# Performance work log

Hardware: AMD Instinct MI355X
Metric: run time of the kernel (lower is better)

Reference implementation:

```python
import jax, jax.numpy as jnp
import numpy as np
import math

B, T, E, H = 64, 256, 1024, 16
HD = E // H  # 64
EPS = 1e-5


def layernorm(x, g, b):
    mu = jnp.mean(x, axis=-1, keepdims=True)
    var = jnp.mean(jnp.square(x - mu), axis=-1, keepdims=True)
    return (x - mu) * jax.lax.rsqrt(var + EPS) * g + b


def setup_inputs() -> dict:
    key = jax.random.key(0)
    ks = jax.random.split(key, 10)
    s = 0.02
    return {
        "x": jax.random.normal(ks[0], (B, T, E), dtype=jnp.float32),
        "ln1_g": jnp.ones((E,), jnp.float32),
        "ln1_b": jnp.zeros((E,), jnp.float32),
        "wk": jax.random.normal(ks[1], (H, E, HD), jnp.float32) * s,
        "wq": jax.random.normal(ks[2], (H, E, HD), jnp.float32) * s,
        "wv": jax.random.normal(ks[3], (H, E, HD), jnp.float32) * s,
        "w_proj": jax.random.normal(ks[4], (E, E), jnp.float32) * s,
        "b_proj": jnp.zeros((E,), jnp.float32),
        "ln2_g": jnp.ones((E,), jnp.float32),
        "ln2_b": jnp.zeros((E,), jnp.float32),
        "w1": jax.random.normal(ks[5], (E, E), jnp.float32) * s,
        "b1": jnp.zeros((E,), jnp.float32),
        "w2": jax.random.normal(ks[6], (E, E), jnp.float32) * s,
        "b2": jnp.zeros((E,), jnp.float32),
    }


def reference(x, ln1_g, ln1_b, wk, wq, wv, w_proj, b_proj, ln2_g, ln2_b, w1, b1, w2, b2):
    # --- multi-head causal attention on LN1(x) ---
    h = layernorm(x, ln1_g, ln1_b)
    k = jnp.einsum('bte,hed->bhtd', h, wk)
    q = jnp.einsum('bte,hed->bhtd', h, wq)
    v = jnp.einsum('bte,hed->bhtd', h, wv)
    # NOTE: original computes k @ q^T (K.Q^T), not the standard Q.K^T -- kept faithful
    scores = jnp.einsum('bhtd,bhsd->bhts', k, q) / math.sqrt(HD)
    mask = jnp.tril(jnp.ones((T, T), dtype=bool))
    scores = jnp.where(mask, scores, -jnp.inf)
    attn_w = jax.nn.softmax(scores, axis=-1)  # dropout = identity in eval
    attn = jnp.einsum('bhts,bhsd->bhtd', attn_w, v)
    attn = attn.transpose(0, 2, 1, 3).reshape(B, T, E)  # concat heads
    x = x + attn @ w_proj + b_proj
    # --- feed-forward on LN2(x) ---
    h2 = layernorm(x, ln2_g, ln2_b)
    ff = jax.nn.relu(h2 @ w1 + b1) @ w2 + b2
    return x + ff
```

## Files before the change

### kernel.cpp

```cpp
#include <hip/hip_runtime.h>

typedef unsigned int u32;
typedef unsigned short u16;
typedef __attribute__((ext_vector_type(8))) short bf16x8;
typedef __attribute__((ext_vector_type(4))) float f32x4;

#define GLOBAL_AS __attribute__((address_space(1)))
#define LDS_AS    __attribute__((address_space(3)))

#define B_   64
#define T_   256
#define E_   1024
#define H_   16
#define HD_  64
#define NTOK (B_*T_)
#define K_   1024
#define LNEPS 1e-5f

__device__ __forceinline__ u16 f2bf(float f){
  u32 x = __float_as_uint(f);
  u32 r = x + 0x7fffu + ((x >> 16) & 1u);
  return (u16)(r >> 16);
}
__device__ __forceinline__ u16 f2bf_trunc(float f){
  return (u16)(__float_as_uint(f) >> 16);
}
__device__ __forceinline__ u32 pack2(float a, float b){
  return (u32)f2bf(a) | ((u32)f2bf(b) << 16);
}

__device__ __forceinline__ void gload16(const u16* g, u16* l){
  __builtin_amdgcn_global_load_lds((const GLOBAL_AS void*)g, (LDS_AS void*)l, 16, 0, 0);
}

__global__ __launch_bounds__(256) void ln_bf16_kernel(
    const float* __restrict__ x, const float* __restrict__ g,
    const float* __restrict__ b, u16* __restrict__ o)
{
  int lane  = threadIdx.x & 63;
  int token = (blockIdx.x << 2) + (threadIdx.x >> 6);
  const float4* xr = (const float4*)(x + (size_t)token * E_);
  float4 v[4];
  float s = 0.f, ss = 0.f;
  #pragma unroll
  for (int i = 0; i < 4; ++i){
    v[i] = xr[lane + 64 * i];
    s += v[i].x + v[i].y + v[i].z + v[i].w;
    ss = fmaf(v[i].x, v[i].x, fmaf(v[i].y, v[i].y,
         fmaf(v[i].z, v[i].z, fmaf(v[i].w, v[i].w, ss))));
  }
  #pragma unroll
  for (int off = 32; off > 0; off >>= 1){
    s  += __shfl_xor(s,  off);
    ss += __shfl_xor(ss, off);
  }
  float mu   = s * (1.f / E_);
  float var  = ss * (1.f / E_) - mu * mu;
  float rstd = rsqrtf(var + LNEPS);
  const float4* gr = (const float4*)g;
  const float4* br = (const float4*)b;
  uint2* orow = (uint2*)(o + (size_t)token * E_);
  #pragma unroll
  for (int i = 0; i < 4; ++i){
    float4 gg = gr[lane + 64 * i], bb = br[lane + 64 * i];
    float y0 = (v[i].x - mu) * rstd * gg.x + bb.x;
    float y1 = (v[i].y - mu) * rstd * gg.y + bb.y;
    float y2 = (v[i].z - mu) * rstd * gg.z + bb.z;
    float y3 = (v[i].w - mu) * rstd * gg.w + bb.w;
    orow[lane + 64 * i] = make_uint2(pack2(y0, y1), pack2(y2, y3));
  }
}

__global__ __launch_bounds__(256) void convq_kernel(
    const float* __restrict__ wk, const float* __restrict__ wq,
    const float* __restrict__ wv, u16* __restrict__ o)
{
  __shared__ float tile[64 * 68];
  const int zh = blockIdx.x, z = zh >> 4, h = zh & 15;
  const int k0 = blockIdx.y << 6;
  const float* w = (z == 0 ? wk : z == 1 ? wq : wv) + (size_t)h * (E_ * HD_);
  const int t = threadIdx.x;
  {
    int kr = t >> 2, d0 = (t & 3) << 4;
    const float4* src = (const float4*)(w + (size_t)(k0 + kr) * HD_ + d0);
    #pragma unroll
    for (int i = 0; i < 4; ++i)
      *(float4*)(tile + kr * 68 + d0 + 4 * i) = src[i];
  }
  __syncthreads();
  {
    const size_t nb32 = (size_t)zh * 32 + (k0 >> 5);
    #pragma unroll
    for (int u = 0; u < 2; ++u) {
      int cid = t * 2 + u;
      int dd = cid >> 3, kc = cid & 7;
      u32 wd[4];
      #pragma unroll
      for (int e2 = 0; e2 < 4; ++e2)
        wd[e2] = pack2(tile[(kc * 8 + 2 * e2) * 68 + dd],
                       tile[(kc * 8 + 2 * e2 + 1) * 68 + dd]);
      u16* dst = o + (nb32 + (kc >> 2)) * 2048 + (size_t)(dd >> 4) * 512
                   + (size_t)(((kc & 3) << 4) + (dd & 15)) * 8;
      *(uint4*)dst = make_uint4(wd[0], wd[1], wd[2], wd[3]);
    }
  }
}

__global__ __launch_bounds__(256) void convt3_kernel(
    const float* __restrict__ wp, const float* __restrict__ w1,
    const float* __restrict__ w2, u16* __restrict__ op,
    u16* __restrict__ o1, u16* __restrict__ o2)
{
  __shared__ float tile[64 * 68];
  const int z = blockIdx.z;
  const float* w = (z == 0 ? wp : z == 1 ? w1 : w2);
  u16* o = (z == 0 ? op : z == 1 ? o1 : o2);
  const int n0 = blockIdx.x << 6, k0 = blockIdx.y << 6;
  const int t = threadIdx.x;
  {
    int kr = t >> 2, nn = (t & 3) << 4;
    const float4* src = (const float4*)(w + (size_t)(k0 + kr) * E_ + n0 + nn);
    #pragma unroll
    for (int i = 0; i < 4; ++i)
      *(float4*)(tile + kr * 68 + nn + 4 * i) = src[i];
  }
  __syncthreads();
  {
    const size_t nb32 = (size_t)(n0 >> 6) * 32 + (k0 >> 5);
    #pragma unroll
    for (int u = 0; u < 2; ++u) {
      int cid = t * 2 + u;
      int dd = cid >> 3, kc = cid & 7;
      u32 wd[4];
      #pragma unroll
      for (int e2 = 0; e2 < 4; ++e2)
        wd[e2] = pack2(tile[(kc * 8 + 2 * e2) * 68 + dd],
                       tile[(kc * 8 + 2 * e2 + 1) * 68 + dd]);
      u16* dst = o + (nb32 + (kc >> 2)) * 2048 + (size_t)(dd >> 4) * 512
                   + (size_t)(((kc & 3) << 4) + (dd & 15)) * 8;
      *(uint4*)dst = make_uint4(wd[0], wd[1], wd[2], wd[3]);
    }
  }
}

#define MF4(I, AV, BV)                                                               \
  acc[I][0] = __builtin_amdgcn_mfma_f32_16x16x32_bf16(AV, BV[0], acc[I][0], 0, 0, 0);\
  acc[I][1] = __builtin_amdgcn_mfma_f32_16x16x32_bf16(AV, BV[1], acc[I][1], 0, 0, 0);\
  acc[I][2] = __builtin_amdgcn_mfma_f32_16x16x32_bf16(AV, BV[2], acc[I][2], 0, 0, 0);\
  acc[I][3] = __builtin_amdgcn_mfma_f32_16x16x32_bf16(AV, BV[3], acc[I][3], 0, 0, 0);

#define BLOADS(BV, SS) {                                                      \
    const u16* bp_ = Bp + (size_t)(SS) * 2048;                                \
    BV[0] = *(const bf16x8*)(bp_);                                            \
    BV[1] = *(const bf16x8*)(bp_ + 512);                                      \
    BV[2] = *(const bf16x8*)(bp_ + 1024);                                     \
    BV[3] = *(const bf16x8*)(bp_ + 1536);                                     \
  }

#define MSLICE2(SLOT, NSLOT, KA, DO_STAGE, DO_NXT, DO_BL, BS, ACUR, ATMP, ANXT, BV, BNV, VM) { \
    const u16* As_ = lds + (SLOT) * 4096;                                     \
          \
    ATMP[0] = *(const bf16x8*)(As_ + aoffb + 1024);                           \
    ATMP[1] = *(const bf16x8*)(As_ + aoffb + 1536);                           \
    if (DO_STAGE) {                                                           \
      u16* d_ = lds + (((SLOT) + 3) & 3) * 4096;                              \
      gload16(Ag0 + (KA), d_ + tid * 8);                                      \
      gload16(Ag1 + (KA), d_ + 2048 + tid * 8);                               \
    }                                                                         \
    __builtin_amdgcn_s_setprio(1);                                            \
    MF4(0, ACUR[0], BV) MF4(1, ACUR[1], BV)                                   \
    __builtin_amdgcn_s_setprio(0);                                            \
             \
    if (DO_NXT) {                                                             \
      const u16* An_ = lds + (NSLOT) * 4096;                                  \
      ANXT[0] = *(const bf16x8*)(An_ + aoffb);                                \
      ANXT[1] = *(const bf16x8*)(An_ + aoffb + 512);                          \
    }                                                                         \
    __builtin_amdgcn_s_setprio(1);                                            \
    MF4(2, ATMP[0], BV) MF4(3, ATMP[1], BV)                                   \
    __builtin_amdgcn_s_setprio(0);                                            \
    if (DO_BL) { BLOADS(BNV, BS) }                                            \
    VM;                                                                       \
    __builtin_amdgcn_s_barrier();                                             \
    __builtin_amdgcn_sched_barrier(0);                                        \
    asm volatile("" ::: "memory");                                            \
  }

#define VM10 asm volatile("s_waitcnt vmcnt(10)" ::: "memory")
#define VM8  asm volatile("s_waitcnt vmcnt(8)"  ::: "memory")
#define VM4  asm volatile("s_waitcnt vmcnt(4)"  ::: "memory")

template<int MODE>
__global__ __launch_bounds__(256, 3) void mgemm_kernel(
    const u16* __restrict__ A, const u16* __restrict__ Bt,
    const float* __restrict__ bias, const float* __restrict__ resid,
    float* __restrict__ Cf, u16* __restrict__ Cb, u16* __restrict__ Cb2)
{
  __shared__ __align__(16) u16 lds[16384];

  const int tid = threadIdx.x, lane = tid & 63, wid = tid >> 6;
  const int wm = wid >> 1, wn = wid & 1;
  const int l15 = lane & 15, quad = lane >> 4;

  const int b = (int)blockIdx.x;
  const int xcd = b & 7, ib = b >> 3;
  const int mloc = ib & 15, ntile = ib >> 4;
  const int row0 = (xcd * 16 + mloc) << 7;
  const int col0 = ntile << 7;

  const int sc   = (tid & 7) ^ ((tid >> 3) & 7);
  const int srow = 2 * (tid >> 3) + (sc >> 2);
  const int skof = (sc & 3) << 3;
  const u16* Ag0 = A + (size_t)(row0 + srow) * K_ + skof;
  const u16* Ag1 = Ag0 + (size_t)64 * K_;

  const int rhalf = l15 >> 1;
  const int cph   = ((((l15 & 1) << 2) | quad) ^ rhalf);
  const int aoffb = wm * 2048 + rhalf * 64 + cph * 8;

  const u16* Bp = Bt + (size_t)((col0 >> 6) + wn) * 65536 + lane * 8;

  f32x4 acc[4][4];
  #pragma unroll
  for (int i = 0; i < 4; ++i)
    #pragma unroll
    for (int j = 0; j < 4; ++j)
      acc[i][j] = (f32x4){0.f, 0.f, 0.f, 0.f};

  bf16x8 aA[2], aB[2], aT[2], bE[4], bO[4];

  #pragma unroll
  for (int t3 = 0; t3 < 3; ++t3) {
    u16* d_ = lds + t3 * 4096;
    gload16(Ag0 + t3 * 32, d_ + tid * 8);
    gload16(Ag1 + t3 * 32, d_ + 2048 + tid * 8);
  }
  BLOADS(bE, 0)
  BLOADS(bO, 1)
  asm volatile("s_waitcnt vmcnt(10)" ::: "memory");
  __builtin_amdgcn_s_barrier();
  __builtin_amdgcn_sched_barrier(0);
  asm volatile("" ::: "memory");

  aA[0] = *(const bf16x8*)(lds + aoffb);
  aA[1] = *(const bf16x8*)(lds + aoffb + 512);

  #pragma unroll 1
  for (int s = 0; s < 28; s += 2) {
    MSLICE2(s & 3, (s + 1) & 3, (s + 3) * 32, 1, 1, 1, s + 2, aA, aT, aB, bE, bE, VM10)
    MSLICE2((s + 1) & 3, (s + 2) & 3, (s + 4) * 32, 1, 1, 1, s + 3, aB, aT, aA, bO, bO, VM10)
  }
  MSLICE2(0, 1, 31 * 32, 1, 1, 1, 30, aA, aT, aB, bE, bE, VM10)
  MSLICE2(1, 2, 0,       0, 1, 1, 31, aB, aT, aA, bO, bO, VM8 )
  MSLICE2(2, 3, 0,       0, 1, 0, 0,  aA, aT, aB, bE, bE, VM4 )
  MSLICE2(3, 0, 0,       0, 0, 0, 0,  aB, aT, aA, bO, bO, (void)0)

  if (MODE == 1 || MODE == 3) {
    const int rbase = row0 + wm * 64;
    #pragma unroll
    for (int j = 0; j < 4; ++j) {
      const int n = col0 + wn * 64 + j * 16 + l15;
      const float bn = bias[n];
      #pragma unroll
      for (int i = 0; i < 4; ++i)
        #pragma unroll
        for (int r = 0; r < 4; ++r) {
          const int row = rbase + i * 16 + quad * 4 + r;
          const size_t idx = (size_t)row * E_ + n;
          float v = acc[i][j][r] + bn;
          if (MODE == 1) Cf[idx] = v + resid[idx];
          else           Cf[idx] = v + Cf[idx];
        }
    }
    return;
  }

  u16* ep = lds + wid * 4096;
  const int nb0 = col0 + wn * 64;

  if (MODE == 2) {
    #pragma unroll
    for (int j = 0; j < 4; ++j) {
      const float bn = bias[nb0 + j * 16 + l15];
      #pragma unroll
      for (int i = 0; i < 4; ++i)
        #pragma unroll
        for (int r = 0; r < 4; ++r)
          ep[(i*16 + quad*4 + r) * 64 + j*16 + l15] =
              f2bf(fmaxf(acc[i][j][r] + bn, 0.f));
    }
    const int rbase = row0 + wm * 64;
    #pragma unroll
    for (int it = 0; it < 8; ++it) {
      const int tl = it * 8 + (lane >> 3), c = lane & 7;
      uint4 v = *(const uint4*)(ep + tl * 64 + c * 8);
      *(uint4*)(Cb + (size_t)(rbase + tl) * E_ + nb0 + c * 8) = v;
    }
    return;
  }

  const int z = nb0 >> 10, hh = (nb0 >> 6) & 15;
  const int rows0 = row0 + wm * 64;
  const int bb = rows0 >> 8, tb = rows0 & 255;
  if (z < 2) {
    #pragma unroll
    for (int i = 0; i < 4; ++i)
      #pragma unroll
      for (int j = 0; j < 4; ++j)
        #pragma unroll
        for (int r = 0; r < 4; ++r)
          ep[(i*16 + quad*4 + r) * 64 + j*16 + l15] = f2bf(acc[i][j][r]);
    u16* out = (z == 0 ? Cb : Cb2) + ((size_t)(bb * H_ + hh) * T_ + tb) * HD_;
    #pragma unroll
    for (int it = 0; it < 8; ++it) {
      const int tl = it * 8 + (lane >> 3), c = lane & 7;
      uint4 v = *(const uint4*)(ep + tl * 64 + c * 8);
      *(uint4*)(out + (size_t)tl * HD_ + c * 8) = v;
    }
  } else {
    #pragma unroll
    for (int i = 0; i < 4; ++i)
      #pragma unroll
      for (int j = 0; j < 4; ++j)
        #pragma unroll
        for (int r = 0; r < 4; ++r) {
          const int tl = i*16 + quad*4 + r, d = j*16 + l15;
          const int cs = (tl >> 3) ^ (d & 7);
          ep[d * 64 + cs * 8 + (tl & 7)] = f2bf(acc[i][j][r]);
        }
    u16* out = (u16*)Cf + ((size_t)(bb * H_ + hh) * HD_) * T_;
    #pragma unroll
    for (int it = 0; it < 8; ++it) {
      const int d = it * 8 + (lane >> 3), c = lane & 7;
      const int cs = c ^ (d & 7);
      uint4 v = *(const uint4*)(ep + d * 64 + cs * 8);
      *(uint4*)(out + (size_t)d * T_ + tb + c * 8) = v;
    }
  }
}

__global__ __launch_bounds__(256, 1) void fattn_kernel(
    const u16* __restrict__ kk_, const u16* __restrict__ qq_,
    const u16* __restrict__ vt_, u16* __restrict__ out)
{
  __shared__ __align__(16) u16 Pb[4][64 * 72];
  const int tid = threadIdx.x, lane = tid & 63, wv = tid >> 6;
  const int bh = blockIdx.x;
  const int tblk = wv;
  const int l15 = lane & 15, quad = lane >> 4;
  const u16* kb  = kk_ + (size_t)bh * (T_ * HD_);
  const u16* qb  = qq_ + (size_t)bh * (T_ * HD_);
  const u16* vtb = vt_ + (size_t)bh * (HD_ * T_);
  u16* Pw = Pb[wv];

  bf16x8 kf[4][2];
  #pragma unroll
  for (int i = 0; i < 4; ++i)
    #pragma unroll
    for (int c = 0; c < 2; ++c)
      kf[i][c] = *(const bf16x8*)(kb + (size_t)(tblk*64 + i*16 + l15) * HD_ + c*32 + quad*8);

  bf16x8 qf[4][2];
  #pragma unroll
  for (int j = 0; j < 4; ++j)
    #pragma unroll
    for (int c = 0; c < 2; ++c)
      qf[j][c] = *(const bf16x8*)(qb + (size_t)(j*16 + l15) * HD_ + c*32 + quad*8);

  f32x4 o[4][4];
  float mrow[4][4], lrow[4][4];
  #pragma unroll
  for (int i = 0; i < 4; ++i) {
    #pragma unroll
    for (int j = 0; j < 4; ++j) o[i][j] = (f32x4){0.f, 0.f, 0.f, 0.f};
    #pragma unroll
    for (int r = 0; r < 4; ++r) { mrow[i][r] = -1e30f; lrow[i][r] = 0.f; }
  }

  for (int sb = 0; sb <= tblk; ++sb) {
    f32x4 S[4][4];
    __builtin_amdgcn_s_setprio(1);
    #pragma unroll
    for (int j = 0; j < 4; ++j)
      #pragma unroll
      for (int i = 0; i < 4; ++i) {
        f32x4 t0 = __builtin_amdgcn_mfma_f32_16x16x32_bf16(kf[i][0], qf[j][0],
                       (f32x4){0.f,0.f,0.f,0.f}, 0, 0, 0);
        S[i][j] = __builtin_amdgcn_mfma_f32_16x16x32_bf16(kf[i][1], qf[j][1], t0, 0, 0, 0);
      }
    __builtin_amdgcn_s_setprio(0);
    if (sb < tblk) {
      #pragma unroll
      for (int j = 0; j < 4; ++j)
        #pragma unroll
        for (int c = 0; c < 2; ++c)
          qf[j][c] = *(const bf16x8*)(qb + (size_t)((sb+1)*64 + j*16 + l15) * HD_ + c*32 + quad*8);
    }
    bf16x8 vf[4][2];
    #pragma unroll
    for (int jd = 0; jd < 4; ++jd)
      #pragma unroll
      for (int c = 0; c < 2; ++c)
        vf[jd][c] = *(const bf16x8*)(vtb + (size_t)(jd*16 + l15) * T_ + sb*64 + c*32 + quad*8);
    #pragma unroll
    for (int i = 0; i < 4; ++i)
      #pragma unroll
      for (int j = 0; j < 4; ++j)
        #pragma unroll
        for (int r = 0; r < 4; ++r) {
          float val = S[i][j][r] * 0.125f;
          if (sb == tblk) {
            int tl = i*16 + quad*4 + r, sl = j*16 + l15;
            if (sl > tl) val = -1e30f;
          }
          S[i][j][r] = val;
        }
    #pragma unroll
    for (int i = 0; i < 4; ++i)
      #pragma unroll
      for (int r = 0; r < 4; ++r) {
        float mx = fmaxf(fmaxf(S[i][0][r], S[i][1][r]), fmaxf(S[i][2][r], S[i][3][r]));
        #pragma unroll
        for (int msk = 1; msk < 16; msk <<= 1) mx = fmaxf(mx, __shfl_xor(mx, msk));
        float mn = fmaxf(mrow[i][r], mx);
        float al = __expf(mrow[i][r] - mn);
        mrow[i][r] = mn;
        float sm = 0.f;
        #pragma unroll
        for (int j = 0; j < 4; ++j) {
          float p = __expf(S[i][j][r] - mn);
          S[i][j][r] = p;
          sm += p;
        }
        #pragma unroll
        for (int msk = 1; msk < 16; msk <<= 1) sm += __shfl_xor(sm, msk);
        lrow[i][r] = lrow[i][r] * al + sm;
        #pragma unroll
        for (int jd = 0; jd < 4; ++jd) o[i][jd][r] *= al;
      }
    #pragma unroll
    for (int i = 0; i < 4; ++i)
      #pragma unroll
      for (int j = 0; j < 4; ++j)
        #pragma unroll
        for (int r = 0; r < 4; ++r)
          Pw[(i*16 + quad*4 + r) * 72 + j*16 + l15] = f2bf_trunc(S[i][j][r]);
    bf16x8 pf[4][2];
    #pragma unroll
    for (int i = 0; i < 4; ++i)
      #pragma unroll
      for (int c = 0; c < 2; ++c)
        pf[i][c] = *(const bf16x8*)(Pw + (i*16 + l15) * 72 + c*32 + quad*8);
    __builtin_amdgcn_s_setprio(1);
    #pragma unroll
    for (int jd = 0; jd < 4; ++jd)
      #pragma unroll
      for (int i = 0; i < 4; ++i) {
        f32x4 t0 = __builtin_amdgcn_mfma_f32_16x16x32_bf16(pf[i][0], vf[jd][0], o[i][jd], 0, 0, 0);
        o[i][jd] = __builtin_amdgcn_mfma_f32_16x16x32_bf16(pf[i][1], vf[jd][1], t0, 0, 0, 0);
      }
    __builtin_amdgcn_s_setprio(0);
  }

  #pragma unroll
  for (int i = 0; i < 4; ++i)
    #pragma unroll
    for (int r = 0; r < 4; ++r) {
      float inv = 1.0f / lrow[i][r];
      #pragma unroll
      for (int jd = 0; jd < 4; ++jd)
        Pw[(i*16 + quad*4 + r) * 72 + jd*16 + l15] = f2bf(o[i][jd][r] * inv);
    }
  {
    const int b = bh >> 4, h = bh & 15;
    const uint4* pr = (const uint4*)(Pw + lane * 72);
    uint4* og = (uint4*)(out + ((size_t)(b * T_ + tblk*64 + lane)) * E_ + h * HD_);
    #pragma unroll
    for (int k = 0; k < 8; ++k) og[k] = pr[k];
  }
}

extern "C" void kernel_launch(void* const* d_in, const int* in_sizes, int n_in,
                              void* d_out, int out_size, void* d_ws, size_t ws_size,
                              hipStream_t stream) {
  const float* x     = (const float*)d_in[0];
  const float* ln1g  = (const float*)d_in[1];
  const float* ln1b  = (const float*)d_in[2];
  const float* wk    = (const float*)d_in[3];
  const float* wq    = (const float*)d_in[4];
  const float* wv    = (const float*)d_in[5];
  const float* wproj = (const float*)d_in[6];
  const float* bproj = (const float*)d_in[7];
  const float* ln2g  = (const float*)d_in[8];
  const float* ln2b  = (const float*)d_in[9];
  const float* w1    = (const float*)d_in[10];
  const float* b1    = (const float*)d_in[11];
  const float* w2    = (const float*)d_in[12];
  const float* b2    = (const float*)d_in[13];
  float* outp = (float*)d_out;

  char* ws = (char*)d_ws;
  const size_t MB = 1024 * 1024;
  u16* wqkvT  = (u16*)(ws);
  u16* wprojT = (u16*)(ws + 6 * MB);
  u16* w1T    = (u16*)(ws + 8 * MB);
  u16* w2T    = (u16*)(ws + 10 * MB);
  u16* hb     = (u16*)(ws + 16 * MB);
  u16* kbuf   = (u16*)(ws + 48 * MB);
  u16* qbuf   = (u16*)(ws + 80 * MB);
  u16* vtbuf  = (u16*)d_out;

  convq_kernel<<<dim3(48, 16), 256, 0, stream>>>(wk, wq, wv, wqkvT);
  convt3_kernel<<<dim3(16, 16, 3), 256, 0, stream>>>(wproj, w1, w2, wprojT, w1T, w2T);

  ln_bf16_kernel<<<NTOK/4, 256, 0, stream>>>(x, ln1g, ln1b, hb);
  mgemm_kernel<0><<<3072, 256, 0, stream>>>(
      hb, wqkvT, nullptr, nullptr, (float*)vtbuf, kbuf, qbuf);
  fattn_kernel<<<B_*H_, 256, 0, stream>>>(kbuf, qbuf, vtbuf, hb);
  mgemm_kernel<1><<<1024, 256, 0, stream>>>(
      hb, wprojT, bproj, x, outp, nullptr, nullptr);
  ln_bf16_kernel<<<NTOK/4, 256, 0, stream>>>(outp, ln2g, ln2b, kbuf);
  mgemm_kernel<2><<<1024, 256, 0, stream>>>(
      kbuf, w1T, b1, nullptr, nullptr, qbuf, nullptr);
  mgemm_kernel<3><<<1024, 256, 0, stream>>>(
      qbuf, w2T, b2, nullptr, outp, nullptr, nullptr);
}
```

Before: 526.0 us.

## Transpose attention scores, fold scale into Wq, keep P in registers

The flash-attention kernel now computes S^T so each lane owns one query row. That lets softmax row reductions use two cross-lane shuffles instead of four, and it lets P feed a 16x16x16 bf16 MFMA directly from registers without an LDS round trip. The 1/sqrt(d) scale is folded into the Wq conversion, removing a per-element multiply. The grid is reshaped so each wave handles a different (batch, head) with blocks ordered longest-causal-first, and launch bounds allow two blocks per CU. The risks are the extra register pressure from two blocks per CU and lower per-instruction throughput of the 16x16x16 MFMA.

```diff
diff --git a/kernel.cpp b/kernel.cpp
--- a/kernel.cpp
+++ b/kernel.cpp
@@ -3,7 +3,14 @@
 typedef unsigned int u32;
 typedef unsigned short u16;
 typedef __attribute__((ext_vector_type(8))) short bf16x8;
+typedef __attribute__((ext_vector_type(4))) short bf16x4;
 typedef __attribute__((ext_vector_type(4))) float f32x4;
+
+#if defined(__has_builtin)
+#if __has_builtin(__builtin_amdgcn_mfma_f32_16x16x16bf16_1k)
+#define HAVE_MFMA16_1K 1
+#endif
+#endif
 
 #define GLOBAL_AS __attribute__((address_space(1)))
 #define LDS_AS    __attribute__((address_space(3)))
@@ -79,6 +86,7 @@
   const int zh = blockIdx.x, z = zh >> 4, h = zh & 15;
   const int k0 = blockIdx.y << 6;
   const float* w = (z == 0 ? wk : z == 1 ? wq : wv) + (size_t)h * (E_ * HD_);
+  const float qs = (z == 1) ? 0.125f : 1.0f;
   const int t = threadIdx.x;
   {
     int kr = t >> 2, d0 = (t & 3) << 4;
@@ -97,8 +105,8 @@
       u32 wd[4];
       #pragma unroll
       for (int e2 = 0; e2 < 4; ++e2)
-        wd[e2] = pack2(tile[(kc * 8 + 2 * e2) * 68 + dd],
-                       tile[(kc * 8 + 2 * e2 + 1) * 68 + dd]);
+        wd[e2] = pack2(qs * tile[(kc * 8 + 2 * e2) * 68 + dd],
+                       qs * tile[(kc * 8 + 2 * e2 + 1) * 68 + dd]);
       u16* dst = o + (nb32 + (kc >> 2)) * 2048 + (size_t)(dd >> 4) * 512
                    + (size_t)(((kc & 3) << 4) + (dd & 15)) * 8;
       *(uint4*)dst = make_uint4(wd[0], wd[1], wd[2], wd[3]);
@@ -159,7 +167,6 @@
 
 #define MSLICE2(SLOT, NSLOT, KA, DO_STAGE, DO_NXT, DO_BL, BS, ACUR, ATMP, ANXT, BV, BNV, VM) { \
     const u16* As_ = lds + (SLOT) * 4096;                                     \
-          \
     ATMP[0] = *(const bf16x8*)(As_ + aoffb + 1024);                           \
     ATMP[1] = *(const bf16x8*)(As_ + aoffb + 1536);                           \
     if (DO_STAGE) {                                                           \
@@ -170,7 +177,6 @@
     __builtin_amdgcn_s_setprio(1);                                            \
     MF4(0, ACUR[0], BV) MF4(1, ACUR[1], BV)                                   \
     __builtin_amdgcn_s_setprio(0);                                            \
-             \
     if (DO_NXT) {                                                             \
       const u16* An_ = lds + (NSLOT) * 4096;                                  \
       ANXT[0] = *(const bf16x8*)(An_ + aoffb);                                \
@@ -339,14 +345,14 @@
   }
 }
 
-__global__ __launch_bounds__(256, 1) void fattn_kernel(
+__global__ __launch_bounds__(256, 2) void fattn_kernel(
     const u16* __restrict__ kk_, const u16* __restrict__ qq_,
     const u16* __restrict__ vt_, u16* __restrict__ out)
 {
   __shared__ __align__(16) u16 Pb[4][64 * 72];
   const int tid = threadIdx.x, lane = tid & 63, wv = tid >> 6;
-  const int bh = blockIdx.x;
-  const int tblk = wv;
+  const int bh = blockIdx.x * 4 + wv;
+  const int tblk = 3 - (int)blockIdx.y;
   const int l15 = lane & 15, quad = lane >> 4;
   const u16* kb  = kk_ + (size_t)bh * (T_ * HD_);
   const u16* qb  = qq_ + (size_t)bh * (T_ * HD_);
@@ -367,26 +373,25 @@
     for (int c = 0; c < 2; ++c)
       qf[j][c] = *(const bf16x8*)(qb + (size_t)(j*16 + l15) * HD_ + c*32 + quad*8);
 
-  f32x4 o[4][4];
-  float mrow[4][4], lrow[4][4];
+  f32x4 accT[4][4];
+  float mrow[4], lrow[4];
   #pragma unroll
   for (int i = 0; i < 4; ++i) {
     #pragma unroll
-    for (int j = 0; j < 4; ++j) o[i][j] = (f32x4){0.f, 0.f, 0.f, 0.f};
-    #pragma unroll
-    for (int r = 0; r < 4; ++r) { mrow[i][r] = -1e30f; lrow[i][r] = 0.f; }
+    for (int jd = 0; jd < 4; ++jd) accT[jd][i] = (f32x4){0.f, 0.f, 0.f, 0.f};
+    mrow[i] = -1e30f; lrow[i] = 0.f;
   }
 
   for (int sb = 0; sb <= tblk; ++sb) {
-    f32x4 S[4][4];
+    f32x4 ST[4][4];
     __builtin_amdgcn_s_setprio(1);
     #pragma unroll
     for (int j = 0; j < 4; ++j)
       #pragma unroll
       for (int i = 0; i < 4; ++i) {
-        f32x4 t0 = __builtin_amdgcn_mfma_f32_16x16x32_bf16(kf[i][0], qf[j][0],
+        f32x4 t0 = __builtin_amdgcn_mfma_f32_16x16x32_bf16(qf[j][0], kf[i][0],
                        (f32x4){0.f,0.f,0.f,0.f}, 0, 0, 0);
-        S[i][j] = __builtin_amdgcn_mfma_f32_16x16x32_bf16(kf[i][1], qf[j][1], t0, 0, 0, 0);
+        ST[j][i] = __builtin_amdgcn_mfma_f32_16x16x32_bf16(qf[j][1], kf[i][1], t0, 0, 0, 0);
       }
     __builtin_amdgcn_s_setprio(0);
     if (sb < tblk) {
@@ -396,81 +401,109 @@
         for (int c = 0; c < 2; ++c)
           qf[j][c] = *(const bf16x8*)(qb + (size_t)((sb+1)*64 + j*16 + l15) * HD_ + c*32 + quad*8);
     }
+#ifdef HAVE_MFMA16_1K
+    bf16x4 vv[4][4];
+    #pragma unroll
+    for (int j = 0; j < 4; ++j)
+      #pragma unroll
+      for (int jd = 0; jd < 4; ++jd)
+        vv[j][jd] = *(const bf16x4*)(vtb + (size_t)(jd*16 + l15) * T_ + sb*64 + j*16 + quad*4);
+#else
     bf16x8 vf[4][2];
     #pragma unroll
     for (int jd = 0; jd < 4; ++jd)
       #pragma unroll
       for (int c = 0; c < 2; ++c)
         vf[jd][c] = *(const bf16x8*)(vtb + (size_t)(jd*16 + l15) * T_ + sb*64 + c*32 + quad*8);
-    #pragma unroll
-    for (int i = 0; i < 4; ++i)
+#endif
+    if (sb == tblk) {
       #pragma unroll
       for (int j = 0; j < 4; ++j)
         #pragma unroll
+        for (int i = 0; i < 4; ++i)
+          #pragma unroll
+          for (int r = 0; r < 4; ++r)
+            if (j*16 + quad*4 + r > i*16 + l15) ST[j][i][r] = -1e30f;
+    }
+    #pragma unroll
+    for (int i = 0; i < 4; ++i) {
+      float mx = ST[0][i][0];
+      #pragma unroll
+      for (int j = 0; j < 4; ++j)
+        #pragma unroll
+        for (int r = 0; r < 4; ++r) mx = fmaxf(mx, ST[j][i][r]);
+      mx = fmaxf(mx, __shfl_xor(mx, 16));
+      mx = fmaxf(mx, __shfl_xor(mx, 32));
+      float mn = fmaxf(mrow[i], mx);
+      float al = __expf(mrow[i] - mn);
+      mrow[i] = mn;
+      float sm = 0.f;
+      #pragma unroll
+      for (int j = 0; j < 4; ++j)
+        #pragma unroll
         for (int r = 0; r < 4; ++r) {
-          float val = S[i][j][r] * 0.125f;
-          if (sb == tblk) {
-            int tl = i*16 + quad*4 + r, sl = j*16 + l15;
-            if (sl > tl) val = -1e30f;
-          }
-          S[i][j][r] = val;
-        }
-    #pragma unroll
-    for (int i = 0; i < 4; ++i)
-      #pragma unroll
-      for (int r = 0; r < 4; ++r) {
-        float mx = fmaxf(fmaxf(S[i][0][r], S[i][1][r]), fmaxf(S[i][2][r], S[i][3][r]));
-        #pragma unroll
-        for (int msk = 1; msk < 16; msk <<= 1) mx = fmaxf(mx, __shfl_xor(mx, msk));
-        float mn = fmaxf(mrow[i][r], mx);
-        float al = __expf(mrow[i][r] - mn);
-        mrow[i][r] = mn;
-        float sm = 0.f;
-        #pragma unroll
-        for (int j = 0; j < 4; ++j) {
-          float p = __expf(S[i][j][r] - mn);
-          S[i][j][r] = p;
+          float p = __expf(ST[j][i][r] - mn);
+          ST[j][i][r] = p;
           sm += p;
         }
-        #pragma unroll
-        for (int msk = 1; msk < 16; msk <<= 1) sm += __shfl_xor(sm, msk);
-        lrow[i][r] = lrow[i][r] * al + sm;
-        #pragma unroll
-        for (int jd = 0; jd < 4; ++jd) o[i][jd][r] *= al;
-      }
+      sm += __shfl_xor(sm, 16);
+      sm += __shfl_xor(sm, 32);
+      lrow[i] = lrow[i] * al + sm;
+      #pragma unroll
+      for (int jd = 0; jd < 4; ++jd) accT[jd][i] = accT[jd][i] * al;
+    }
+#ifdef HAVE_MFMA16_1K
+    #pragma unroll
+    for (int j = 0; j < 4; ++j) {
+      bf16x4 pfj[4];
+      #pragma unroll
+      for (int i = 0; i < 4; ++i)
+        pfj[i] = (bf16x4){(short)f2bf_trunc(ST[j][i][0]), (short)f2bf_trunc(ST[j][i][1]),
+                          (short)f2bf_trunc(ST[j][i][2]), (short)f2bf_trunc(ST[j][i][3])};
+      __builtin_amdgcn_s_setprio(1);
+      #pragma unroll
+      for (int jd = 0; jd < 4; ++jd)
+        #pragma unroll
+        for (int i = 0; i < 4; ++i)
+          accT[jd][i] = __builtin_amdgcn_mfma_f32_16x16x16bf16_1k(
+              vv[j][jd], pfj[i], accT[jd][i], 0, 0, 0);
+      __builtin_amdgcn_s_setprio(0);
+    }
+#else
+    #pragma unroll
+    for (int j = 0; j < 4; ++j)
+      #pragma unroll
+      for (int i = 0; i < 4; ++i)
+        #pragma unroll
+        for (int r = 0; r < 4; ++r)
+          Pw[(i*16 + l15) * 72 + j*16 + quad*4 + r] = f2bf_trunc(ST[j][i][r]);
+    bf16x8 pfB[4][2];
     #pragma unroll
     for (int i = 0; i < 4; ++i)
       #pragma unroll
-      for (int j = 0; j < 4; ++j)
-        #pragma unroll
-        for (int r = 0; r < 4; ++r)
-          Pw[(i*16 + quad*4 + r) * 72 + j*16 + l15] = f2bf_trunc(S[i][j][r]);
-    bf16x8 pf[4][2];
-    #pragma unroll
-    for (int i = 0; i < 4; ++i)
-      #pragma unroll
       for (int c = 0; c < 2; ++c)
-        pf[i][c] = *(const bf16x8*)(Pw + (i*16 + l15) * 72 + c*32 + quad*8);
+        pfB[i][c] = *(const bf16x8*)(Pw + (i*16 + l15) * 72 + c*32 + quad*8);
     __builtin_amdgcn_s_setprio(1);
     #pragma unroll
     for (int jd = 0; jd < 4; ++jd)
       #pragma unroll
       for (int i = 0; i < 4; ++i) {
-        f32x4 t0 = __builtin_amdgcn_mfma_f32_16x16x32_bf16(pf[i][0], vf[jd][0], o[i][jd], 0, 0, 0);
-        o[i][jd] = __builtin_amdgcn_mfma_f32_16x16x32_bf16(pf[i][1], vf[jd][1], t0, 0, 0, 0);
+        f32x4 t0 = __builtin_amdgcn_mfma_f32_16x16x32_bf16(vf[jd][0], pfB[i][0], accT[jd][i], 0, 0, 0);
+        accT[jd][i] = __builtin_amdgcn_mfma_f32_16x16x32_bf16(vf[jd][1], pfB[i][1], t0, 0, 0, 0);
       }
     __builtin_amdgcn_s_setprio(0);
-  }
-
-  #pragma unroll
-  for (int i = 0; i < 4; ++i)
-    #pragma unroll
-    for (int r = 0; r < 4; ++r) {
-      float inv = 1.0f / lrow[i][r];
-      #pragma unroll
-      for (int jd = 0; jd < 4; ++jd)
-        Pw[(i*16 + quad*4 + r) * 72 + jd*16 + l15] = f2bf(o[i][jd][r] * inv);
-    }
+#endif
+  }
+
+  #pragma unroll
+  for (int i = 0; i < 4; ++i) {
+    float inv = 1.0f / lrow[i];
+    #pragma unroll
+    for (int jd = 0; jd < 4; ++jd)
+      #pragma unroll
+      for (int r = 0; r < 4; ++r)
+        Pw[(i*16 + l15) * 72 + jd*16 + quad*4 + r] = f2bf(accT[jd][i][r] * inv);
+  }
   {
     const int b = bh >> 4, h = bh & 15;
     const uint4* pr = (const uint4*)(Pw + lane * 72);
@@ -516,7 +549,7 @@
   ln_bf16_kernel<<<NTOK/4, 256, 0, stream>>>(x, ln1g, ln1b, hb);
   mgemm_kernel<0><<<3072, 256, 0, stream>>>(
       hb, wqkvT, nullptr, nullptr, (float*)vtbuf, kbuf, qbuf);
-  fattn_kernel<<<B_*H_, 256, 0, stream>>>(kbuf, qbuf, vtbuf, hb);
+  fattn_kernel<<<dim3(B_*H_/4, 4), 256, 0, stream>>>(kbuf, qbuf, vtbuf, hb);
   mgemm_kernel<1><<<1024, 256, 0, stream>>>(
       hb, wprojT, bproj, x, outp, nullptr, nullptr);
   ln_bf16_kernel<<<NTOK/4, 256, 0, stream>>>(outp, ln2g, ln2b, kbuf);
```

Result: faster. 478.5 us (-9.0%).
